# Kernel optimization log

Measured on AMD Instinct MI355X. Metric: run time of the kernel, lower is better.

## Reference

```python
import jax, jax.numpy as jnp
import numpy as np

D = 1024
N_HEAD = 16
D_HEAD = D // N_HEAD
EPS = 1e-6


def setup_inputs() -> dict:
    key = jax.random.key(0)
    k1, k2, k3 = jax.random.split(key, 3)
    x = jax.random.normal(k1, (4, 1024, D), dtype=jnp.float32)
    # Linear weights stored as (in, out); y = x @ W
    Wqkv = jax.random.normal(k2, (D, 3 * D), dtype=jnp.float32) * (1.0 / np.sqrt(D))
    Wo = jax.random.normal(k3, (D, D), dtype=jnp.float32) * (1.0 / np.sqrt(D))
    scale_q = jnp.ones((D_HEAD,), dtype=jnp.float32)
    scale_k = jnp.ones((D_HEAD,), dtype=jnp.float32)
    return {"x": x, "Wqkv": Wqkv, "Wo": Wo, "scale_q": scale_q, "scale_k": scale_k}


def _rmsnorm_global(x, scale):
    # NOTE: faithful to source: mean over ALL elements (scalar RMS), not per-vector.
    rms = jnp.sqrt(jnp.mean(x * x))
    return (x / (rms + EPS)) * scale  # scale broadcasts over last dim (d_head)


def reference(x, Wqkv, Wo, scale_q, scale_k):
    b, s, d = x.shape
    qkv = x @ Wqkv  # (b, s, 3d)
    q, k, v = jnp.split(qkv, 3, axis=-1)
    q = q.reshape(b, s, N_HEAD, D_HEAD)
    k = k.reshape(b, s, N_HEAD, D_HEAD)
    v = v.reshape(b, s, N_HEAD, D_HEAD)
    q = _rmsnorm_global(q, scale_q)
    k = _rmsnorm_global(k, scale_k)
    # NOTE: no 1/sqrt(d_head) scaling, no mask (faithful to source)
    attn = jnp.einsum('bqhd,bkhd->bhqk', q, k)
    attn = jax.nn.softmax(attn, axis=-1)
    z = jnp.einsum('bhqk,bkhd->bqhd', attn, v)
    z = z.reshape(b, s, d)
    return z @ Wo
```

## Files before the change

kernel.cpp:

```cpp
#include <hip/hip_runtime.h>

typedef float f32x4 __attribute__((ext_vector_type(4)));
typedef short bf16x8 __attribute__((ext_vector_type(8)));
typedef _Float16 f16x8 __attribute__((ext_vector_type(8)));
typedef unsigned short u16;

__device__ __forceinline__ u16 f2bf(float f) {
  unsigned int u = __float_as_uint(f);
  u = u + 0x7fffu + ((u >> 16) & 1u);
  return (u16)(u >> 16);
}
__device__ __forceinline__ float bf2f(u16 h) {
  return __uint_as_float(((unsigned int)h) << 16);
}
__device__ __forceinline__ u16 f2h(float f) {
  _Float16 h = (_Float16)f;
  union { _Float16 h; u16 u; } cv;
  cv.h = h;
  return cv.u;
}

typedef unsigned int as1_uint __attribute__((address_space(1)));
typedef unsigned int as3_uint __attribute__((address_space(3)));
__device__ __forceinline__ void gl_lds16(const void* g, void* l) {
  __builtin_amdgcn_global_load_lds((as1_uint*)g, (as3_uint*)l, 16, 0, 0);
}


__global__ __launch_bounds__(256) void conv_x_kernel(const float* __restrict__ x,
                                                     u16* __restrict__ Xp) {
  const int g = blockIdx.x * 256 + threadIdx.x;
  const int o = g * 8;
  const int slab = o >> 17;
  const int rem = o & 131071;
  const int kstep = rem >> 12;
  const int rem2 = rem & 4095;
  const int r = rem2 >> 5;
  const int cp = (rem2 & 31) >> 3;
  const int c = cp ^ ((r >> 1) & 3);
  const int s = slab * 128 + r;
  const int k = kstep * 32 + c * 8;
  const float4 v0 = *(const float4*)&x[(size_t)s * 1024 + k];
  const float4 v1 = *(const float4*)&x[(size_t)s * 1024 + k + 4];
  ushort4 a, b;
  a.x = f2h(v0.x); a.y = f2h(v0.y); a.z = f2h(v0.z); a.w = f2h(v0.w);
  b.x = f2h(v1.x); b.y = f2h(v1.y); b.z = f2h(v1.z); b.w = f2h(v1.w);
  *(ushort4*)&Xp[o] = a;
  *(ushort4*)&Xp[o + 4] = b;
}

__global__ __launch_bounds__(256) void conv_w_kernel(
    const float* __restrict__ src, int ncols, u16* __restrict__ dst) {
  __shared__ float tl[64][132];
  const int t = threadIdx.x;
  const int slab = blockIdx.x, kg = blockIdx.y;
  const int n0 = slab * 128, k0 = kg * 64;
#pragma unroll
  for (int i = 0; i < 8; i++) {
    const int fidx = i * 256 + t;
    const int r = fidx >> 5, c4 = (fidx & 31) * 4;
    *(float4*)&tl[r][c4] = *(const float4*)&src[(size_t)(k0 + r) * ncols + n0 + c4];
  }
  __syncthreads();
  const size_t base = (size_t)slab * 131072 + (size_t)(kg * 2) * 4096;
#pragma unroll
  for (int i = 0; i < 4; i++) {
    const int g = i * 256 + t;
    const int img = g >> 9, ci = g & 511;
    const int r = ci >> 2, cp = ci & 3;
    const int c = cp ^ ((r >> 1) & 3);
    const int klc = img * 32 + c * 8;
    ushort4 h0, h1;
    float v[8];
#pragma unroll
    for (int e = 0; e < 8; e++) v[e] = tl[klc + e][r];
    h0.x = f2h(v[0]); h0.y = f2h(v[1]); h0.z = f2h(v[2]); h0.w = f2h(v[3]);
    h1.x = f2h(v[4]); h1.y = f2h(v[5]); h1.z = f2h(v[6]); h1.w = f2h(v[7]);
    *(ushort4*)&dst[base + g * 8] = h0;
    *(ushort4*)&dst[base + g * 8 + 4] = h1;
  }
}

__global__ __launch_bounds__(512, 2) void gemm_qkv_kernel(
    const u16* __restrict__ Xp, const u16* __restrict__ Wp,
    u16* __restrict__ qf, u16* __restrict__ kf, u16* __restrict__ vT,
    const float* __restrict__ scale_q, const float* __restrict__ scale_k,
    float* __restrict__ sums) {
  __shared__ u16 SA[2][4][4096];
  __shared__ u16 SB[2][4][4096];
  const int tid = threadIdx.x, wv = tid >> 6, lane = tid & 63;
  const int lm = lane & 15, quad = lane >> 4;
  const int wvM = wv >> 2, wvN = wv & 3;
  const int L = blockIdx.x;
  const int xcd = L & 7, idx = L >> 3;
  const int bmT = (xcd & 3) * 4 + (idx & 3);
  const int bnT = (xcd >> 2) * 6 + (idx >> 2);
  const bool is_v = (bnT >= 8);
  const int fq = (quad ^ ((lm >> 1) & 3)) * 8;
  const int aOff = lm * 32 + fq;
  const u16* Xg = Xp + (size_t)bmT * 262144;
  const u16* Wg = Wp + (size_t)bnT * 262144;
  int bSub[4];
#pragma unroll
  for (int n = 0; n < 4; n++) {
    const int wn = wvN * 64 + n * 16;
    bSub[n] = ((wn >> 7) * 4096) + (wn & 127) * 32;
  }
  const u16* Ard = is_v ? &SA[0][0][0] : &SB[0][0][0];
  const u16* Brd = is_v ? &SB[0][0][0] : &SA[0][0][0];

  const f32x4 z4 = {0.f, 0.f, 0.f, 0.f};
  f32x4 acc[8][4];
#pragma unroll
  for (int i = 0; i < 8; i++)
#pragma unroll
    for (int j = 0; j < 4; j++) acc[i][j] = z4;

#define VMCNT4() asm volatile("s_waitcnt vmcnt(4)" ::: "memory")
#define VMCNT0() asm volatile("s_waitcnt vmcnt(0)" ::: "memory")
#define LGKM0() asm volatile("s_waitcnt lgkmcnt(0)" ::: "memory")
#define CFENCE() asm volatile("" ::: "memory")

#define QSTAGE(tt, nb, k2, sl)                                               \
  do {                                                                       \
    const size_t go_ = (size_t)(sl)*131072 + (size_t)(2 * (tt) + (k2)) * 4096\
                       + wv * 512 + lane * 8;                                \
    gl_lds16(Xg + go_, &SA[nb][(k2)*2 + (sl)][wv * 512]);                    \
    gl_lds16(Wg + go_, &SB[nb][(k2)*2 + (sl)][wv * 512]);                    \
  } while (0)

#define READ_A(BUF, k2, mq)                                                  \
  _Pragma("unroll")                                                          \
  for (int i = 0; i < 4; i++)                                                \
    afr[i] = *(const f16x8*)&Ard[(BUF)*16384 + ((k2)*2 + wvM) * 4096 +       \
                                 ((mq)*4 + i) * 512 + aOff];
#define READ_B(BUF, k2)                                                      \
  _Pragma("unroll")                                                          \
  for (int n = 0; n < 4; n++)                                                \
    bfr[n] = *(const f16x8*)&Brd[(BUF)*16384 + (k2)*8192 + bSub[n] + aOff];
#define MFMA16(mq)                                                           \
  _Pragma("unroll")                                                          \
  for (int i = 0; i < 4; i++)                                                \
    _Pragma("unroll")                                                        \
    for (int n = 0; n < 4; n++)                                              \
      acc[(mq)*4 + i][n] = __builtin_amdgcn_mfma_f32_16x16x32_f16(           \
          afr[i], bfr[n], acc[(mq)*4 + i][n], 0, 0, 0);

#define PH_TOP(BUF, k2, mq)                                                  \
  __builtin_amdgcn_s_barrier();                                              \
  CFENCE();                                                                  \
  READ_A(BUF, k2, mq)
#define PH_BOT(mq)                                                           \
  LGKM0();                                                                   \
  __builtin_amdgcn_sched_barrier(0);                                         \
  __builtin_amdgcn_s_setprio(1);                                             \
  MFMA16(mq);                                                                \
  __builtin_amdgcn_s_setprio(0)

#define KTILE(BUF, NBUF, t, DOSTAGE, W2)                                     \
  do {                                                                       \
    f16x8 afr[4], bfr[4];                                                    \
                                                   \
    VMCNT4();                                                                \
    PH_TOP(BUF, 0, 0);                                                       \
    READ_B(BUF, 0);                                                          \
    if (DOSTAGE) QSTAGE((t) + 1, NBUF, 0, 0);                                \
    PH_BOT(0);                                                               \
                                                  \
    PH_TOP(BUF, 0, 1);                                                       \
    if (DOSTAGE) QSTAGE((t) + 1, NBUF, 0, 1);                                \
    PH_BOT(1);                                                               \
                                                   \
    W2;                                                                      \
    PH_TOP(BUF, 1, 0);                                                       \
    READ_B(BUF, 1);                                                          \
    if (DOSTAGE) QSTAGE((t) + 1, NBUF, 1, 0);                                \
    PH_BOT(0);                                                               \
                                                  \
    PH_TOP(BUF, 1, 1);                                                       \
    if (DOSTAGE) QSTAGE((t) + 1, NBUF, 1, 1);                                \
    PH_BOT(1);                                                               \
  } while (0)

  QSTAGE(0, 0, 0, 0);
  QSTAGE(0, 0, 0, 1);
  QSTAGE(0, 0, 1, 0);
  QSTAGE(0, 0, 1, 1);
#pragma unroll 1
  for (int t = 0; t < 14; t += 2) {
    KTILE(0, 1, t, true, VMCNT4());
    KTILE(1, 0, t + 1, true, VMCNT4());
  }
  KTILE(0, 1, 14, true, VMCNT4());
  KTILE(1, 0, 15, false, VMCNT0());
#undef KTILE
#undef PH_TOP
#undef PH_BOT
#undef READ_A
#undef READ_B
#undef MFMA16
#undef QSTAGE

  const int bn = bnT * 256, bm = bmT * 256;
  if (!is_v) {
    const bool is_k = (bnT >= 4);
    u16* dst = is_k ? kf : qf;
    float ss = 0.f;
#pragma unroll
    for (int mi = 0; mi < 8; mi++) {
      const int col0 = bn + wvM * 128 + mi * 16 + quad * 4;
      const int hh = (col0 >> 6) & 15, d0 = col0 & 63;
      const int dhi = d0 >> 5, cc = (d0 & 31) >> 3, eo = d0 & 7;
      float sc[4] = {1.f, 1.f, 1.f, 1.f};
      if (is_k) {
        const float4 sq = *(const float4*)&scale_q[d0];
        const float4 sk = *(const float4*)&scale_k[d0];
        sc[0] = sq.x * sk.x; sc[1] = sq.y * sk.y;
        sc[2] = sq.z * sk.z; sc[3] = sq.w * sk.w;
      }
#pragma unroll
      for (int ni = 0; ni < 4; ni++) {
        const int s = bm + wvN * 64 + ni * 16 + lm;
        const int b = s >> 10, sl = s & 1023, st = sl >> 6, r = sl & 63;
        const size_t off = ((size_t)((b * 16 + hh) * 16 + st)) * 4096 +
                           dhi * 2048 + r * 32 + ((cc ^ ((r >> 1) & 3)) * 8) + eo;
        ushort4 h4;
#pragma unroll
        for (int i = 0; i < 4; i++) {
          const float a = acc[mi][ni][i];
          ss += a * a;
          const u16 hv = f2h(a * sc[i]);
          if (i == 0) h4.x = hv;
          else if (i == 1) h4.y = hv;
          else if (i == 2) h4.z = hv;
          else h4.w = hv;
        }
        *(ushort4*)&dst[off] = h4;
      }
    }
#pragma unroll
    for (int m = 32; m >= 1; m >>= 1) ss += __shfl_xor(ss, m, 64);
    if (lane == 0) atomicAdd(&sums[is_k ? 1 : 0], ss);
  } else {
#pragma unroll
    for (int ni = 0; ni < 4; ni++) {
      const int col = (bn - 2048) + wvN * 64 + ni * 16 + lm;
      const int d = col & 63, hh = col >> 6;
#pragma unroll
      for (int mi = 0; mi < 8; mi++) {
        const int s0 = bm + wvM * 128 + mi * 16 + quad * 4;
        const int b = s0 >> 10, sl = s0 & 1023, st = sl >> 6;
        const int sh = (sl & 63) >> 5, cc = (sl & 31) >> 3, eo = sl & 7;
        const size_t off = ((size_t)((b * 16 + hh) * 16 + st)) * 4096 +
                           sh * 2048 + d * 32 + ((cc ^ ((d >> 1) & 3)) * 8) + eo;
        ushort4 v4;
        v4.x = f2bf(acc[mi][ni][0]);
        v4.y = f2bf(acc[mi][ni][1]);
        v4.z = f2bf(acc[mi][ni][2]);
        v4.w = f2bf(acc[mi][ni][3]);
        *(ushort4*)&vT[off] = v4;
      }
    }
  }
#undef VMCNT4
#undef VMCNT0
#undef LGKM0
#undef CFENCE
}

__global__ __launch_bounds__(256) void attn_kernel(
    const u16* __restrict__ qf, const u16* __restrict__ kf,
    const u16* __restrict__ vT, const float* __restrict__ sums,
    u16* __restrict__ z) {
  __shared__ u16 Ks0[4096], Vs0[4096], Ks1[4096], Vs1[4096];
  __shared__ u16 pb[4][2][16][64];
  const int tid = threadIdx.x, wv = tid >> 6, lane = tid & 63;
  const int lm = lane & 15, quad = lane >> 4;
  const int fq = (quad ^ ((lm >> 1) & 3)) * 8;
  const int L = blockIdx.x;
  const int xcd = L & 7, idx = L >> 3;
  const int qt8 = idx & 7, p = idx >> 3;
  const int pair = xcd * 8 + p;
  const int hh = pair & 15, b = pair >> 4;
  const float inv_rq = 1.f / (sqrtf(sums[0] * (1.f / 4194304.f)) + 1e-6f);
  const float inv_rk = 1.f / (sqrtf(sums[1] * (1.f / 4194304.f)) + 1e-6f);
  const float cs = inv_rq * inv_rk;
  const size_t hb = ((size_t)(b * 16 + hh)) * 65536;
  const u16* Kg = kf + hb;
  const u16* Vg = vT + hb;
  const int dof = wv * 1024;

  f16x8 aF[2][2];
#pragma unroll
  for (int qs = 0; qs < 2; qs++) {
    const int soff = wv * 32 + qs * 16;
    const size_t qb = hb + (size_t)(qt8 * 2 + (soff >> 6)) * 4096 +
                      (size_t)((soff & 63) + lm) * 32 + fq;
    aF[qs][0] = *(const f16x8*)&qf[qb];
    aF[qs][1] = *(const f16x8*)&qf[qb + 2048];
  }
  const f32x4 zz = {0.f, 0.f, 0.f, 0.f};
  f32x4 zac[2][4];
#pragma unroll
  for (int qs = 0; qs < 2; qs++)
#pragma unroll
    for (int dt = 0; dt < 4; dt++) zac[qs][dt] = zz;
  float rs[2] = {0.f, 0.f};

#define AISSUE(it, Ks, Vs)                                    \
  do {                                                        \
    const size_t tb_ = (size_t)(it) * 4096;                   \
    gl_lds16(Kg + tb_ + dof + lane * 8, &Ks[dof]);            \
    gl_lds16(Kg + tb_ + dof + 512 + lane * 8, &Ks[dof + 512]);\
    gl_lds16(Vg + tb_ + dof + lane * 8, &Vs[dof]);            \
    gl_lds16(Vg + tb_ + dof + 512 + lane * 8, &Vs[dof + 512]);\
  } while (0)

#define ATTN_BODY(it, Ks, Vs, Kn, Vn, do_issue)                               \
  do {                                                                        \
                                         \
    f16x8 kf0[4], kf1[4];                                                     \
    bf16x8 bv[2][4];                                                          \
_Pragma("unroll")                                                             \
    for (int nt = 0; nt < 4; nt++) {                                          \
      const int ro = (nt * 16 + lm) * 32 + fq;                                \
      kf0[nt] = *(const f16x8*)&Ks[ro];                                       \
      kf1[nt] = *(const f16x8*)&Ks[2048 + ro];                                \
    }                                                                         \
_Pragma("unroll")                                                             \
    for (int ch = 0; ch < 2; ch++)                                            \
_Pragma("unroll")                                                             \
      for (int dt = 0; dt < 4; dt++)                                          \
        bv[ch][dt] = *(const bf16x8*)&Vs[ch * 2048 + (dt * 16 + lm) * 32 + fq];\
    if (do_issue) AISSUE((it) + 1, Kn, Vn);                                   \
               \
_Pragma("unroll")                                                             \
    for (int qs = 0; qs < 2; qs++) {                                          \
_Pragma("unroll")                                                             \
      for (int nt = 0; nt < 4; nt++) {                                        \
        f32x4 c = zz;                                                         \
        c = __builtin_amdgcn_mfma_f32_16x16x32_f16(kf0[nt], aF[qs][0], c, 0, 0, 0);\
        c = __builtin_amdgcn_mfma_f32_16x16x32_f16(kf1[nt], aF[qs][1], c, 0, 0, 0);\
        const int k4 = nt * 4 + quad;                                         \
        const int sw = (k4 & 8) | ((k4 ^ lm) & 7);                            \
        ushort4 pw;                                                           \
        float p0 = __expf(c[0] * cs - 60.f);                                  \
        float p1 = __expf(c[1] * cs - 60.f);                                  \
        float p2 = __expf(c[2] * cs - 60.f);                                  \
        float p3 = __expf(c[3] * cs - 60.f);                                  \
        rs[qs] += (p0 + p1) + (p2 + p3);                                      \
        pw.x = f2bf(p0); pw.y = f2bf(p1); pw.z = f2bf(p2); pw.w = f2bf(p3);   \
        *(ushort4*)&pb[wv][qs][lm][sw * 4] = pw;                              \
      }                                                                       \
    }                                                                         \
           \
_Pragma("unroll")                                                             \
    for (int ch = 0; ch < 2; ch++) {                                          \
_Pragma("unroll")                                                             \
      for (int qs = 0; qs < 2; qs++) {                                        \
        const int k4a = ch * 8 + quad * 2, k4b = k4a + 1;                     \
        const ushort4 lo4 =                                                   \
            *(const ushort4*)&pb[wv][qs][lm][((k4a & 8) | ((k4a ^ lm) & 7)) * 4];\
        const ushort4 hi4 =                                                   \
            *(const ushort4*)&pb[wv][qs][lm][((k4b & 8) | ((k4b ^ lm) & 7)) * 4];\
        bf16x8 ap;                                                            \
        ap[0] = (short)lo4.x; ap[1] = (short)lo4.y;                           \
        ap[2] = (short)lo4.z; ap[3] = (short)lo4.w;                           \
        ap[4] = (short)hi4.x; ap[5] = (short)hi4.y;                           \
        ap[6] = (short)hi4.z; ap[7] = (short)hi4.w;                           \
_Pragma("unroll")                                                             \
        for (int dt = 0; dt < 4; dt++)                                        \
          zac[qs][dt] = __builtin_amdgcn_mfma_f32_16x16x32_bf16(              \
              bv[ch][dt], ap, zac[qs][dt], 0, 0, 0);                          \
      }                                                                       \
    }                                                                         \
  } while (0)

  AISSUE(0, Ks0, Vs0);
  for (int it = 0; it < 16; it += 2) {
    __syncthreads();
    ATTN_BODY(it, Ks0, Vs0, Ks1, Vs1, true);
    __syncthreads();
    ATTN_BODY(it + 1, Ks1, Vs1, Ks0, Vs0, (it + 2 < 16));
  }
#undef AISSUE
#undef ATTN_BODY

#pragma unroll
  for (int qs = 0; qs < 2; qs++) {
    rs[qs] += __shfl_xor(rs[qs], 16, 64);
    rs[qs] += __shfl_xor(rs[qs], 32, 64);
  }
  const int slab = b * 8 + qt8;
#pragma unroll
  for (int qs = 0; qs < 2; qs++) {
    const float inv = 1.f / rs[qs];
    const int r = wv * 32 + qs * 16 + lm;
#pragma unroll
    for (int dt = 0; dt < 4; dt++) {
      const int kstep = hh * 2 + (dt >> 1);
      const int d0 = dt * 16 + quad * 4;
      const int cc = (d0 & 31) >> 3, eo = d0 & 7;
      const size_t off = ((size_t)(slab * 32 + kstep)) * 4096 + r * 32 +
                         ((cc ^ ((r >> 1) & 3)) * 8) + eo;
      ushort4 o;
      o.x = f2h(zac[qs][dt][0] * inv);
      o.y = f2h(zac[qs][dt][1] * inv);
      o.z = f2h(zac[qs][dt][2] * inv);
      o.w = f2h(zac[qs][dt][3] * inv);
      *(ushort4*)&z[off] = o;
    }
  }
}

__global__ __launch_bounds__(256) void gemm_o_kernel(const u16* __restrict__ Wop,
                                                     const u16* __restrict__ zp,
                                                     float* __restrict__ out) {
  __shared__ u16 As0[4096], Bs0[4096], As1[4096], Bs1[4096];
  const int tid = threadIdx.x, wv = tid >> 6, lane = tid & 63;
  const int lm = lane & 15, quad = lane >> 4;
  const int wr = (wv >> 1) * 64, wc = (wv & 1) * 64;
  const int fq = (quad ^ ((lm >> 1) & 3)) * 8;
  const int L = blockIdx.x;
  const int xcd = L & 7, idx = L >> 3;
  const int rr = idx & 7, cc8 = idx >> 3;
  const int zpS = (xcd & 3) * 8 + rr;
  const int woS = (xcd >> 2) * 4 + cc8;
  const u16* Ag = Wop + (size_t)woS * 131072;
  const u16* Bg = zp + (size_t)zpS * 131072;
  const int dof0 = (wv * 2) * 512, dof1 = (wv * 2 + 1) * 512;
  const f32x4 z4 = {0.f, 0.f, 0.f, 0.f};
  f32x4 acc[4][4];
#pragma unroll
  for (int i = 0; i < 4; i++)
#pragma unroll
    for (int j = 0; j < 4; j++) acc[i][j] = z4;

#define ISSUE(t, As, Bs)                                   \
  do {                                                     \
    const size_t tb_ = (size_t)(t) * 4096;                 \
    gl_lds16(Ag + tb_ + dof0 + lane * 8, &As[dof0]);       \
    gl_lds16(Ag + tb_ + dof1 + lane * 8, &As[dof1]);       \
    gl_lds16(Bg + tb_ + dof0 + lane * 8, &Bs[dof0]);       \
    gl_lds16(Bg + tb_ + dof1 + lane * 8, &Bs[dof1]);       \
  } while (0)
#define GBODY(As, Bs)                                                     \
  do {                                                                    \
    f16x8 afr[4], bfr[4];                                                 \
_Pragma("unroll")                                                         \
    for (int mi = 0; mi < 4; mi++)                                        \
      afr[mi] = *(const f16x8*)&As[(wr + mi * 16 + lm) * 32 + fq];        \
_Pragma("unroll")                                                         \
    for (int ni = 0; ni < 4; ni++)                                        \
      bfr[ni] = *(const f16x8*)&Bs[(wc + ni * 16 + lm) * 32 + fq];        \
    DO_ISSUE;                                                             \
_Pragma("unroll")                                                         \
    for (int mi = 0; mi < 4; mi++)                                        \
_Pragma("unroll")                                                         \
      for (int ni = 0; ni < 4; ni++)                                      \
        acc[mi][ni] = __builtin_amdgcn_mfma_f32_16x16x32_f16(             \
            afr[mi], bfr[ni], acc[mi][ni], 0, 0, 0);                      \
  } while (0)

  ISSUE(0, As0, Bs0);
  for (int t = 0; t < 32; t += 2) {
    __syncthreads();
#define DO_ISSUE ISSUE(t + 1, As1, Bs1)
    GBODY(As0, Bs0);
#undef DO_ISSUE
    __syncthreads();
#define DO_ISSUE if (t + 2 < 32) ISSUE(t + 2, As0, Bs0)
    GBODY(As1, Bs1);
#undef DO_ISSUE
  }
#undef ISSUE
#undef GBODY

#pragma unroll
  for (int mi = 0; mi < 4; mi++) {
    const int col0 = woS * 128 + wr + mi * 16 + quad * 4;
#pragma unroll
    for (int ni = 0; ni < 4; ni++) {
      const int s = zpS * 128 + wc + ni * 16 + lm;
      const float4 o = {acc[mi][ni][0], acc[mi][ni][1], acc[mi][ni][2],
                        acc[mi][ni][3]};
      *(float4*)&out[(size_t)s * 1024 + col0] = o;
    }
  }
}

extern "C" void kernel_launch(void* const* d_in, const int* in_sizes, int n_in,
                              void* d_out, int out_size, void* d_ws,
                              size_t ws_size, hipStream_t stream) {
  (void)in_sizes; (void)n_in; (void)out_size; (void)ws_size;
  const float* x = (const float*)d_in[0];
  const float* Wqkv = (const float*)d_in[1];
  const float* Wo = (const float*)d_in[2];
  const float* scale_q = (const float*)d_in[3];
  const float* scale_k = (const float*)d_in[4];
  float* out = (float*)d_out;

  char* ws = (char*)d_ws;
  u16* qf = (u16*)(ws + 0);
  u16* kf = (u16*)(ws + 8388608);
  u16* Xp = (u16*)(ws + 16777216);
  u16* vT = (u16*)(ws + 25165824);
  u16* Wp = (u16*)(ws + 33554432);
  u16* zp = Xp;
  u16* Wop = Wp;
  float* sums = (float*)(ws + 39845888);

  conv_x_kernel<<<2048, 256, 0, stream>>>(x, Xp);
  conv_w_kernel<<<dim3(24, 16), 256, 0, stream>>>(Wqkv, 3072, Wp);
  hipMemsetAsync(sums, 0, 2 * sizeof(float), stream);
  gemm_qkv_kernel<<<192, 512, 0, stream>>>(Xp, Wp, qf, kf, vT,
                                           scale_q, scale_k, sums);
  conv_w_kernel<<<dim3(8, 16), 256, 0, stream>>>(Wo, 1024, Wop);
  attn_kernel<<<512, 256, 0, stream>>>(qf, kf, vT, sums, zp);
  gemm_o_kernel<<<256, 256, 0, stream>>>(Wop, zp, out);
}
```

Before: 182.4 us.

## Issue LDS fragment reads before barrier to overlap with wait in QKV GEMM

```diff
diff --git a/kernel.cpp b/kernel.cpp
--- a/kernel.cpp
+++ b/kernel.cpp
@@ -120,6 +120,8 @@
 #define VMCNT0() asm volatile("s_waitcnt vmcnt(0)" ::: "memory")
 #define LGKM0() asm volatile("s_waitcnt lgkmcnt(0)" ::: "memory")
 #define CFENCE() asm volatile("" ::: "memory")
+#define SP1() __builtin_amdgcn_s_setprio(1)
+#define SP0() __builtin_amdgcn_s_setprio(0)
 
 #define QSTAGE(tt, nb, k2, sl)                                               \
   do {                                                                       \
@@ -146,56 +148,70 @@
       acc[(mq)*4 + i][n] = __builtin_amdgcn_mfma_f32_16x16x32_f16(           \
           afr[i], bfr[n], acc[(mq)*4 + i][n], 0, 0, 0);
 
-#define PH_TOP(BUF, k2, mq)                                                  \
+#define PH_WAIT_MFMA(mq)                                                     \
+  CFENCE();                                                                  \
   __builtin_amdgcn_s_barrier();                                              \
   CFENCE();                                                                  \
-  READ_A(BUF, k2, mq)
-#define PH_BOT(mq)                                                           \
   LGKM0();                                                                   \
   __builtin_amdgcn_sched_barrier(0);                                         \
-  __builtin_amdgcn_s_setprio(1);                                             \
+  SP1();                                                                     \
   MFMA16(mq);                                                                \
-  __builtin_amdgcn_s_setprio(0)
-
-#define KTILE(BUF, NBUF, t, DOSTAGE, W2)                                     \
+  SP0()
+
+#define KTILE(BUF, NBUF, t, DOSTAGE, GATE1, GATE3)                           \
   do {                                                                       \
-    f16x8 afr[4], bfr[4];                                                    \
-                                                   \
-    VMCNT4();                                                                \
-    PH_TOP(BUF, 0, 0);                                                       \
-    READ_B(BUF, 0);                                                          \
-    if (DOSTAGE) QSTAGE((t) + 1, NBUF, 0, 0);                                \
-    PH_BOT(0);                                                               \
-                                                  \
-    PH_TOP(BUF, 0, 1);                                                       \
-    if (DOSTAGE) QSTAGE((t) + 1, NBUF, 0, 1);                                \
-    PH_BOT(1);                                                               \
-                                                   \
-    W2;                                                                      \
-    PH_TOP(BUF, 1, 0);                                                       \
-    READ_B(BUF, 1);                                                          \
-    if (DOSTAGE) QSTAGE((t) + 1, NBUF, 1, 0);                                \
-    PH_BOT(0);                                                               \
-                                                  \
-    PH_TOP(BUF, 1, 1);                                                       \
-    if (DOSTAGE) QSTAGE((t) + 1, NBUF, 1, 1);                                \
-    PH_BOT(1);                                                               \
+    f16x8 bfr[4];                                                            \
+    {                                                  \
+      f16x8 afr[4];                                                          \
+      READ_A(BUF, 0, 0);                                                     \
+      READ_B(BUF, 0);                                                        \
+      if (DOSTAGE) QSTAGE((t) + 1, NBUF, 0, 0);                              \
+      PH_WAIT_MFMA(0);                                                       \
+    }                                                                        \
+    {                                                 \
+      f16x8 afr[4];                                                          \
+      READ_A(BUF, 0, 1);                                                     \
+      if (DOSTAGE) QSTAGE((t) + 1, NBUF, 0, 1);                              \
+      GATE1;        \
+      PH_WAIT_MFMA(1);                                                       \
+    }                                                                        \
+    {                                                  \
+      f16x8 afr[4];                                                          \
+      READ_A(BUF, 1, 0);                                                     \
+      READ_B(BUF, 1);                                                        \
+      if (DOSTAGE) QSTAGE((t) + 1, NBUF, 1, 0);                              \
+      PH_WAIT_MFMA(0);                                                       \
+    }                                                                        \
+    {                                                 \
+      f16x8 afr[4];                                                          \
+      READ_A(BUF, 1, 1);                                                     \
+      if (DOSTAGE) QSTAGE((t) + 1, NBUF, 1, 1);                              \
+      GATE3;   \
+      PH_WAIT_MFMA(1);                                                       \
+    }                                                                        \
+    \
+    \
+    CFENCE();                                                                \
+    __builtin_amdgcn_s_barrier();                                            \
+    CFENCE();                                                                \
   } while (0)
 
   QSTAGE(0, 0, 0, 0);
   QSTAGE(0, 0, 0, 1);
   QSTAGE(0, 0, 1, 0);
   QSTAGE(0, 0, 1, 1);
+  VMCNT4();
+  __builtin_amdgcn_s_barrier();
+  CFENCE();
 #pragma unroll 1
   for (int t = 0; t < 14; t += 2) {
-    KTILE(0, 1, t, true, VMCNT4());
-    KTILE(1, 0, t + 1, true, VMCNT4());
-  }
-  KTILE(0, 1, 14, true, VMCNT4());
-  KTILE(1, 0, 15, false, VMCNT0());
+    KTILE(0, 1, t, true, VMCNT4(), VMCNT4());
+    KTILE(1, 0, t + 1, true, VMCNT4(), VMCNT4());
+  }
+  KTILE(0, 1, 14, true, VMCNT4(), VMCNT4());
+  KTILE(1, 0, 15, false, VMCNT0(), (void)0);
 #undef KTILE
-#undef PH_TOP
-#undef PH_BOT
+#undef PH_WAIT_MFMA
 #undef READ_A
 #undef READ_B
 #undef MFMA16
@@ -266,6 +282,8 @@
 #undef VMCNT0
 #undef LGKM0
 #undef CFENCE
+#undef SP1
+#undef SP0
 }
 
 __global__ __launch_bounds__(256) void attn_kernel(
```

Result: no change. 183.4 us (+0.6%).
